# Kernel optimization log

Hardware: AMD Instinct MI355X
Metric: run time of the kernel (lower is better)

Reference implementation:

```python
import jax, jax.numpy as jnp
import numpy as np

HIDDEN = 2048
NUM_HEADS = 16
HEAD_DIM = HIDDEN // NUM_HEADS  # 128
LATENT = HIDDEN // 8            # 256
ROPE_THETA = 100000.0


def setup_inputs() -> dict:
    key = jax.random.key(0)
    ks = jax.random.split(key, 7)
    s = 0.02
    x = jax.random.normal(ks[0], (4, 1024, HIDDEN), dtype=jnp.float32)
    # weights stored as [in, out] (transpose of torch nn.Linear.weight)
    w_q_down = jax.random.normal(ks[1], (HIDDEN, LATENT), dtype=jnp.float32) * s
    w_kv_down = jax.random.normal(ks[2], (HIDDEN, LATENT), dtype=jnp.float32) * s
    w_q_up = jax.random.normal(ks[3], (LATENT, HIDDEN), dtype=jnp.float32) * s
    w_k_up = jax.random.normal(ks[4], (LATENT, HIDDEN), dtype=jnp.float32) * s
    w_v_up = jax.random.normal(ks[5], (LATENT, HIDDEN), dtype=jnp.float32) * s
    w_o = jax.random.normal(ks[6], (HIDDEN, HIDDEN), dtype=jnp.float32) * s
    return {"x": x, "w_q_down": w_q_down, "w_kv_down": w_kv_down,
            "w_q_up": w_q_up, "w_k_up": w_k_up, "w_v_up": w_v_up, "w_o": w_o}


def _rope_cos_sin(seq_len, dtype):
    # Llama rotary: inv_freq over even dims, emb = concat(freqs, freqs)
    inv_freq = 1.0 / (ROPE_THETA ** (jnp.arange(0, HEAD_DIM, 2, dtype=jnp.float32) / HEAD_DIM))
    pos = jnp.arange(seq_len, dtype=jnp.float32)
    freqs = pos[:, None] * inv_freq[None, :]          # [S, D/2]
    emb = jnp.concatenate([freqs, freqs], axis=-1)    # [S, D]
    return jnp.cos(emb).astype(dtype), jnp.sin(emb).astype(dtype)


def _rotate_half(t):
    h = t.shape[-1] // 2
    return jnp.concatenate([-t[..., h:], t[..., :h]], axis=-1)


def reference(x, w_q_down, w_kv_down, w_q_up, w_k_up, w_v_up, w_o):
    B, S, H = x.shape
    q_latent = x @ w_q_down                 # [B,S,latent]
    kv_latent = x @ w_kv_down               # [B,S,latent]
    q = (q_latent @ w_q_up).reshape(B, S, NUM_HEADS, HEAD_DIM)
    k = (kv_latent @ w_k_up).reshape(B, S, NUM_HEADS, HEAD_DIM)
    v = (kv_latent @ w_v_up).reshape(B, S, NUM_HEADS, HEAD_DIM)

    cos, sin = _rope_cos_sin(S, x.dtype)    # [S,D]
    cos = cos[None, :, None, :]             # [1,S,1,D] (unsqueeze_dim=2)
    sin = sin[None, :, None, :]
    q = q * cos + _rotate_half(q) * sin
    k = k * cos + _rotate_half(k) * sin

    # [B,H,S,D]
    q = q.transpose(0, 2, 1, 3)
    k = k.transpose(0, 2, 1, 3)
    v = v.transpose(0, 2, 1, 3)

    scale = 1.0 / jnp.sqrt(jnp.asarray(HEAD_DIM, dtype=x.dtype))
    scores = jnp.einsum('bhqd,bhkd->bhqk', q, k) * scale
    causal = jnp.tril(jnp.ones((S, S), dtype=bool))
    scores = jnp.where(causal[None, None], scores, jnp.finfo(scores.dtype).min)
    probs = jax.nn.softmax(scores, axis=-1)
    attn = jnp.einsum('bhqk,bhkd->bhqd', probs, v)  # [B,H,S,D]
    attn = attn.transpose(0, 2, 1, 3).reshape(B, S, H)
    return attn @ w_o
```

## Files before the change

### kernel.cpp

```cpp
#include <hip/hip_runtime.h>
#include <hip/hip_bf16.h>

typedef unsigned short u16;
typedef unsigned int u32;
typedef __attribute__((ext_vector_type(8))) __bf16 bf16x8;
typedef __attribute__((ext_vector_type(4))) float f32x4;

#define HID 2048
#define NH 16
#define HD 128
#define LAT 256
#define BATCH 4
#define SEQ 1024

__device__ __forceinline__ u16 f2bf(float f) {
  union { float f; u32 u; } v; v.f = f;
  u32 r = v.u + 0x7fffu + ((v.u >> 16) & 1u);
  return (u16)(r >> 16);
}

typedef const __attribute__((address_space(1))) u32 as1_u32;
typedef __attribute__((address_space(3))) u32 as3_u32;

__device__ __forceinline__ void load_lds16(const void* g, void* l) {
  __builtin_amdgcn_global_load_lds((as1_u32*)g, (as3_u32*)l, 16, 0, 0);
}

template<int WM, int WN, int MR, int NR>
__device__ __forceinline__ void gemm_core(const u16* __restrict__ A, const u16* __restrict__ Bt,
    int K, int lda, int ldb, int arow0, int brow0, u16* As, u16* Bs, f32x4 acc[MR][NR]) {
  constexpr int BM = WM * MR * 16, BN = WN * NR * 16;
  constexpr int NW = WM * WN;
  constexpr int ACH = (BM * 32) / 512;
  constexpr int BCH = (BN * 32) / 512;
  const int tid = threadIdx.x;
  const int lane = tid & 63, wave = tid >> 6;
  const int wm = wave % WM, wn = wave / WM;
  const int fr = lane & 15, fq = lane >> 4;

  for (int kt = 0; kt < K; kt += 32) {
    __syncthreads();
    #pragma unroll
    for (int cc = 0; cc < ACH / NW; ++cc) {
      int c = wave + cc * NW;
      int r = c * 16 + (lane >> 2);
      int col = (lane & 3) * 8;
      load_lds16(&A[(size_t)(arow0 + r) * lda + kt + col], &As[c * 512]);
    }
    #pragma unroll
    for (int cc = 0; cc < BCH / NW; ++cc) {
      int c = wave + cc * NW;
      int r = c * 16 + (lane >> 2);
      int col = (lane & 3) * 8;
      load_lds16(&Bt[(size_t)(brow0 + r) * ldb + kt + col], &Bs[c * 512]);
    }
    asm volatile("s_waitcnt vmcnt(0)" ::: "memory");
    __syncthreads();
    bf16x8 af[MR], bfr[NR];
    #pragma unroll
    for (int m = 0; m < MR; ++m)
      af[m] = *(const bf16x8*)&As[(wm * MR * 16 + m * 16 + fr) * 32 + fq * 8];
    #pragma unroll
    for (int n = 0; n < NR; ++n)
      bfr[n] = *(const bf16x8*)&Bs[(wn * NR * 16 + n * 16 + fr) * 32 + fq * 8];
    #pragma unroll
    for (int m = 0; m < MR; ++m)
      #pragma unroll
      for (int n = 0; n < NR; ++n)
        acc[m][n] = __builtin_amdgcn_mfma_f32_16x16x32_bf16(af[m], bfr[n], acc[m][n], 0, 0, 0);
  }
}

__global__ void __launch_bounds__(256) k_cvt(const float* __restrict__ in, u16* __restrict__ o, int n4) {
  int i = blockIdx.x * blockDim.x + threadIdx.x;
  if (i < n4) {
    float4 v = ((const float4*)in)[i];
    union { u16 s[4]; uint2 u; } w;
    w.s[0] = f2bf(v.x); w.s[1] = f2bf(v.y); w.s[2] = f2bf(v.z); w.s[3] = f2bf(v.w);
    ((uint2*)o)[i] = w.u;
  }
}

__global__ void __launch_bounds__(256) k_transpose3(const float* __restrict__ in0,
    const float* __restrict__ in1, const float* __restrict__ in2,
    u16* __restrict__ o0, u16* __restrict__ o1, u16* __restrict__ o2, int R, int C) {
  __shared__ float t[32][33];
  const float* in = blockIdx.z == 0 ? in0 : (blockIdx.z == 1 ? in1 : in2);
  u16* o = blockIdx.z == 0 ? o0 : (blockIdx.z == 1 ? o1 : o2);
  int bx = blockIdx.x * 32, by = blockIdx.y * 32;
  int tx = threadIdx.x, ty = threadIdx.y;
  #pragma unroll
  for (int i = ty; i < 32; i += 8) t[i][tx] = in[(size_t)(by + i) * C + bx + tx];
  __syncthreads();
  #pragma unroll
  for (int i = ty; i < 32; i += 8) o[(size_t)(bx + i) * R + by + tx] = f2bf(t[tx][i]);
}

__global__ void __launch_bounds__(256) k_cossin(float* __restrict__ cosT, float* __restrict__ sinT) {
  int idx = blockIdx.x * 256 + threadIdx.x;
  int s = idx >> 6, d = idx & 63;
  float inv = powf(100000.0f, -(float)d / 64.0f);
  float a = (float)s * inv;
  cosT[idx] = cosf(a);
  sinT[idx] = sinf(a);
}

__global__ void __launch_bounds__(512, 2) k_down(const u16* __restrict__ xb, const u16* __restrict__ wqdT,
    const u16* __restrict__ wkvdT, u16* __restrict__ ql, u16* __restrict__ kvl) {
  __shared__ __align__(16) u16 As[2][128 * 128];
  __shared__ __align__(16) u16 Bs[2][64 * 128];
  const u16* Bt = blockIdx.z ? wkvdT : wqdT;
  u16* out = blockIdx.z ? kvl : ql;
  const int rb = blockIdx.x * 128, cb = blockIdx.y * 64;
  const int tid = threadIdx.x, lane = tid & 63, wave = tid >> 6;
  const int wm = wave & 3, wn = wave >> 2;
  const int fr = lane & 15, fq = lane >> 4;
  const char* Ab = (const char*)xb;
  const char* Bb = (const char*)Bt;
  f32x4 acc[2][2] = {};

  auto stage = [&](int buf, int s) {
    #pragma unroll
    for (int cc = 0; cc < 4; ++cc) {
      int c = wave * 4 + cc;
      int L = c * 1024 + lane * 16;
      int Ls = L ^ (((L >> 8) & 7) << 4);
      int r = Ls >> 8, colb = Ls & 255;
      load_lds16(Ab + (size_t)(rb + r) * 4096 + s * 256 + colb, (char*)As[buf] + c * 1024);
    }
    #pragma unroll
    for (int cc = 0; cc < 2; ++cc) {
      int c = wave * 2 + cc;
      int L = c * 1024 + lane * 16;
      int Ls = L ^ (((L >> 8) & 7) << 4);
      int r = Ls >> 8, colb = Ls & 255;
      load_lds16(Bb + (size_t)(cb + r) * 4096 + s * 256 + colb, (char*)Bs[buf] + c * 1024);
    }
  };

  stage(0, 0);
  int buf = 0;
  for (int s = 0; s < 16; ++s) {
    if (s + 1 < 16) {
      stage(buf ^ 1, s + 1);
      asm volatile("s_waitcnt vmcnt(6)" ::: "memory");
    } else {
      asm volatile("s_waitcnt vmcnt(0)" ::: "memory");
    }
    asm volatile("s_barrier" ::: "memory");

    #pragma unroll
    for (int kk = 0; kk < 4; ++kk) {
      bf16x8 af[2], bfr[2];
      #pragma unroll
      for (int m = 0; m < 2; ++m) {
        int r = wm * 32 + m * 16 + fr;
        af[m] = *(const bf16x8*)((const char*)As[buf] + ((r * 256 + kk * 64 + fq * 16) ^ ((r & 7) << 4)));
      }
      #pragma unroll
      for (int n = 0; n < 2; ++n) {
        int r = wn * 32 + n * 16 + fr;
        bfr[n] = *(const bf16x8*)((const char*)Bs[buf] + ((r * 256 + kk * 64 + fq * 16) ^ ((r & 7) << 4)));
      }
      #pragma unroll
      for (int m = 0; m < 2; ++m)
        #pragma unroll
        for (int n = 0; n < 2; ++n)
          acc[m][n] = __builtin_amdgcn_mfma_f32_16x16x32_bf16(af[m], bfr[n], acc[m][n], 0, 0, 0);
    }

    asm volatile("s_barrier" ::: "memory");
    buf ^= 1;
  }

  #pragma unroll
  for (int m = 0; m < 2; ++m)
    #pragma unroll
    for (int n = 0; n < 2; ++n)
      #pragma unroll
      for (int i = 0; i < 4; ++i)
        out[(size_t)(rb + wm * 32 + m * 16 + fq * 4 + i) * LAT + cb + wn * 32 + n * 16 + fr] =
            f2bf(acc[m][n][i]);
}

__global__ void __launch_bounds__(256) k_up(const u16* __restrict__ ql, const u16* __restrict__ kvl,
    const u16* __restrict__ wquT, const u16* __restrict__ wkuT, const u16* __restrict__ wvuT,
    u16* __restrict__ q, u16* __restrict__ k, u16* __restrict__ vt,
    const float* __restrict__ cosT, const float* __restrict__ sinT) {
  __shared__ __align__(16) u16 As[128 * 32];
  __shared__ __align__(16) u16 Bs[128 * 32];
  const int mode = blockIdx.z;
  const u16* A = (mode == 0) ? ql : kvl;
  const u16* Bt = (mode == 0) ? wquT : (mode == 1 ? wkuT : wvuT);
  const int rb = blockIdx.x * 128;
  const int h = blockIdx.y;
  f32x4 acc[2][8] = {};
  gemm_core<4, 1, 2, 8>(A, Bt, LAT, LAT, LAT, rb, h * HD, As, Bs, acc);
  const int lane = threadIdx.x & 63, wave = threadIdx.x >> 6;
  const int fr = lane & 15, fq = lane >> 4;
  if (mode == 2) {
    #pragma unroll
    for (int m = 0; m < 2; ++m)
      #pragma unroll
      for (int n = 0; n < 8; ++n)
        #pragma unroll
        for (int i = 0; i < 4; ++i) {
          int row = rb + wave * 32 + m * 16 + fq * 4 + i;
          int b = row >> 10, s = row & 1023;
          int sp = (s & ~63) | (((s & 15) << 2) | ((s >> 4) & 3));
          vt[(size_t)((b * NH + h) * HD + n * 16 + fr) * SEQ + sp] = f2bf(acc[m][n][i]);
        }
  } else {
    u16* dst = (mode == 0) ? q : k;
    const float scale = (mode == 0) ? 0.08838834764831845f * 1.4426950408889634f : 1.0f;
    #pragma unroll
    for (int m = 0; m < 2; ++m)
      #pragma unroll
      for (int i = 0; i < 4; ++i) {
        int row = rb + wave * 32 + m * 16 + fq * 4 + i;
        int b = row >> 10, s = row & 1023;
        size_t base = (size_t)((b * NH + h) * SEQ + s) * HD;
        #pragma unroll
        for (int j = 0; j < 4; ++j) {
          int dlo = j * 16 + fr;
          float c = cosT[s * 64 + dlo], sn = sinT[s * 64 + dlo];
          float x1 = acc[m][j][i], x2 = acc[m][j + 4][i];
          dst[base + dlo] = f2bf((x1 * c - x2 * sn) * scale);
          dst[base + dlo + 64] = f2bf((x2 * c + x1 * sn) * scale);
        }
      }
  }
}

__global__ void __launch_bounds__(512, 2) k_attn(const u16* __restrict__ Q, const u16* __restrict__ Kc,
    const u16* __restrict__ Vt, u16* __restrict__ O) {
  __shared__ __align__(16) u16 Ks[2][64 * 128];
  __shared__ __align__(16) u16 Vs[2][128 * 64];
  __shared__ __align__(16) u16 Ps[8][16 * 64];
  const int f = blockIdx.x;
  const int bh = (f & 7) * 8 + (f >> 5);
  const int j = (f >> 3) & 3;
  const int h = bh & (NH - 1), b = bh >> 4;
  const int tid = threadIdx.x, lane = tid & 63, wave = tid >> 6;
  const int fr = lane & 15, fq = lane >> 4;
  const size_t qkb = (size_t)bh * SEQ * HD;
  const char* Kbase = (const char*)Kc + qkb * 2;
  const char* Vbase = (const char*)Vt + (size_t)bh * HD * SEQ * 2;

  const int qx0 = j, qx1 = 7 - j;
  const int nkt0 = 2 * qx0 + 2;
  const int total = 18;

  auto stage = [&](int buf, int t) {
    int kt = (t < nkt0) ? t : (t - nkt0);
    #pragma unroll
    for (int cc = 0; cc < 2; ++cc) {
      int c = wave * 2 + cc;
      int L = c * 1024 + lane * 16;
      int Lk = L ^ (((L >> 8) & 7) << 4);
      load_lds16(Kbase + (size_t)kt * 16384 + Lk, (char*)Ks[buf] + c * 1024);
      int Lv = L ^ (((L >> 7) & 7) << 4);
      int rv = Lv >> 7, colb = Lv & 127;
      load_lds16(Vbase + (size_t)rv * (SEQ * 2) + (size_t)kt * 128 + colb, (char*)Vs[buf] + c * 1024);
    }
  };

  bf16x8 ones;
  #pragma unroll
  for (int z = 0; z < 8; ++z) ones[z] = (__bf16)1.0f;

  bf16x8 qf[4];
  f32x4 ao[8];
  f32x4 lacc;
  int qw = qx0 * 128 + wave * 16;

  auto loadQ = [&]() {
    #pragma unroll
    for (int c = 0; c < 4; ++c)
      qf[c] = *(const bf16x8*)&Q[qkb + (size_t)(qw + fr) * HD + c * 32 + fq * 8];
  };
  auto reset = [&]() {
    f32x4 z = {};
    #pragma unroll
    for (int jj = 0; jj < 8; ++jj) ao[jj] = z;
    lacc = z;
  };
  auto epi = [&]() {
    #pragma unroll
    for (int i = 0; i < 4; ++i) {
      float inv = 1.f / lacc[i];
      int s = qw + fq * 4 + i;
      size_t base = (size_t)(b * SEQ + s) * HID + h * HD;
      #pragma unroll
      for (int jj = 0; jj < 8; ++jj)
        O[base + jj * 16 + fr] = f2bf(ao[jj][i] * inv);
    }
  };

  loadQ();
  reset();
  stage(0, 0);

  int cur = 0;
  for (int t = 0; t < total; ++t) {
    if (t + 1 < total) {
      stage(cur ^ 1, t + 1);
      asm volatile("s_waitcnt vmcnt(4)" ::: "memory");
    } else {
      asm volatile("s_waitcnt vmcnt(0)" ::: "memory");
    }
    asm volatile("s_barrier" ::: "memory");

    if (t == nkt0) {
      epi();
      qw = qx1 * 128 + wave * 16;
      loadQ();
      reset();
    }
    const int ktp = (t < nkt0) ? t : (t - nkt0);
    const int k0 = ktp * 64;
    if (k0 <= qw + 15) {
      f32x4 sc[4] = {};
      #pragma unroll
      for (int c = 0; c < 4; ++c)
        #pragma unroll
        for (int n = 0; n < 4; ++n) {
          int rr = n * 16 + fr;
          int off = (rr * 256 + c * 64 + fq * 16) ^ ((rr & 7) << 4);
          bf16x8 kf = *(const bf16x8*)((const char*)Ks[cur] + off);
          sc[n] = __builtin_amdgcn_mfma_f32_16x16x32_bf16(qf[c], kf, sc[n], 0, 0, 0);
        }

      const bool needmask = (k0 + 63 > qw);
      #pragma unroll
      for (int i = 0; i < 4; ++i) {
        int row = qw + fq * 4 + i;
        float p[4];
        #pragma unroll
        for (int n = 0; n < 4; ++n) {
          float sv = sc[n][i];
          if (needmask) sv = (k0 + n * 16 + fr <= row) ? sv : -1e30f;
          p[n] = exp2f(sv);
        }
        u32 w0, w1;
        asm("v_cvt_pk_bf16_f32 %0, %1, %2" : "=v"(w0) : "v"(p[0]), "v"(p[1]));
        asm("v_cvt_pk_bf16_f32 %0, %1, %2" : "=v"(w1) : "v"(p[2]), "v"(p[3]));
        int prow = fq * 4 + i;
        int o = (prow * 128 + fr * 8) ^ ((prow & 7) << 4);
        *(uint2*)((char*)Ps[wave] + o) = make_uint2(w0, w1);
      }

      bf16x8 pa[2];
      #pragma unroll
      for (int kf = 0; kf < 2; ++kf) {
        int off = (fr * 128 + kf * 64 + fq * 16) ^ ((fr & 7) << 4);
        pa[kf] = *(const bf16x8*)((const char*)Ps[wave] + off);
      }
      lacc = __builtin_amdgcn_mfma_f32_16x16x32_bf16(pa[0], ones, lacc, 0, 0, 0);
      lacc = __builtin_amdgcn_mfma_f32_16x16x32_bf16(pa[1], ones, lacc, 0, 0, 0);
      #pragma unroll
      for (int jj = 0; jj < 8; ++jj)
        #pragma unroll
        for (int kf = 0; kf < 2; ++kf) {
          int rv = jj * 16 + fr;
          int off = (rv * 128 + kf * 64 + fq * 16) ^ ((rv & 7) << 4);
          bf16x8 vf = *(const bf16x8*)((const char*)Vs[cur] + off);
          ao[jj] = __builtin_amdgcn_mfma_f32_16x16x32_bf16(pa[kf], vf, ao[jj], 0, 0, 0);
        }
    }
    asm volatile("s_barrier" ::: "memory");
    cur ^= 1;
  }
  epi();
}

__global__ void __launch_bounds__(512, 2) k_out(const u16* __restrict__ at, const u16* __restrict__ woT,
    float* __restrict__ out) {
  __shared__ __align__(16) u16 As[2][256 * 64];
  __shared__ __align__(16) u16 Bs[2][128 * 64];
  const int rb = blockIdx.x * 256, cb = blockIdx.y * 128;
  const int tid = threadIdx.x, lane = tid & 63, wave = tid >> 6;
  const int wm = wave & 3, wn = wave >> 2;
  const int fr = lane & 15, fq = lane >> 4;
  const char* Ab = (const char*)at;
  const char* Bb = (const char*)woT;
  f32x4 acc[4][4] = {};

  auto stage = [&](int buf, int s) {
    #pragma unroll
    for (int cc = 0; cc < 4; ++cc) {
      int c = wave * 4 + cc;
      int L = c * 1024 + lane * 16;
      int Ls = L ^ (((L >> 7) & 7) << 4);
      int r = Ls >> 7, colb = Ls & 127;
      load_lds16(Ab + (size_t)(rb + r) * 4096 + s * 128 + colb, (char*)As[buf] + c * 1024);
    }
    #pragma unroll
    for (int cc = 0; cc < 2; ++cc) {
      int c = wave * 2 + cc;
      int L = c * 1024 + lane * 16;
      int Ls = L ^ (((L >> 7) & 7) << 4);
      int r = Ls >> 7, colb = Ls & 127;
      load_lds16(Bb + (size_t)(cb + r) * 4096 + s * 128 + colb, (char*)Bs[buf] + c * 1024);
    }
  };

  stage(0, 0);
  int buf = 0;
  for (int s = 0; s < 32; ++s) {
    if (s + 1 < 32) {
      stage(buf ^ 1, s + 1);
      asm volatile("s_waitcnt vmcnt(6)" ::: "memory");
    } else {
      asm volatile("s_waitcnt vmcnt(0)" ::: "memory");
    }
    asm volatile("s_barrier" ::: "memory");

    #pragma unroll
    for (int kk = 0; kk < 2; ++kk) {
      bf16x8 af[4], bfr[4];
      #pragma unroll
      for (int m = 0; m < 4; ++m) {
        int r = wm * 64 + m * 16 + fr;
        af[m] = *(const bf16x8*)((const char*)As[buf] + ((r * 128 + kk * 64 + fq * 16) ^ ((r & 7) << 4)));
      }
      #pragma unroll
      for (int n = 0; n < 4; ++n) {
        int r = wn * 64 + n * 16 + fr;
        bfr[n] = *(const bf16x8*)((const char*)Bs[buf] + ((r * 128 + kk * 64 + fq * 16) ^ ((r & 7) << 4)));
      }
      #pragma unroll
      for (int m = 0; m < 4; ++m)
        #pragma unroll
        for (int n = 0; n < 4; ++n)
          acc[m][n] = __builtin_amdgcn_mfma_f32_16x16x32_bf16(af[m], bfr[n], acc[m][n], 0, 0, 0);
    }

    asm volatile("s_barrier" ::: "memory");
    buf ^= 1;
  }

  #pragma unroll
  for (int m = 0; m < 4; ++m)
    #pragma unroll
    for (int n = 0; n < 4; ++n)
      #pragma unroll
      for (int i = 0; i < 4; ++i)
        out[(size_t)(rb + wm * 64 + m * 16 + fq * 4 + i) * HID + cb + wn * 64 + n * 16 + fr] =
            acc[m][n][i];
}

extern "C" void kernel_launch(void* const* d_in, const int* in_sizes, int n_in,
                              void* d_out, int out_size, void* d_ws, size_t ws_size,
                              hipStream_t stream) {
  const float* x    = (const float*)d_in[0];
  const float* wqd  = (const float*)d_in[1];
  const float* wkvd = (const float*)d_in[2];
  const float* wqu  = (const float*)d_in[3];
  const float* wku  = (const float*)d_in[4];
  const float* wvu  = (const float*)d_in[5];
  const float* wo   = (const float*)d_in[6];
  float* out = (float*)d_out;

  char* p = (char*)d_ws;
  u16* xb    = (u16*)(p + 0);
  u16* at    = xb;
  u16* wqdT  = (u16*)(p + 16777216);
  u16* wkvdT = (u16*)(p + 17825792);
  u16* wquT  = (u16*)(p + 18874368);
  u16* wkuT  = (u16*)(p + 19922944);
  u16* wvuT  = (u16*)(p + 20971520);
  u16* woT   = (u16*)(p + 22020096);
  u16* ql    = (u16*)(p + 30408704);
  u16* kvl   = (u16*)(p + 32505856);
  u16* q     = (u16*)(p + 34603008);
  u16* kk    = (u16*)(p + 51380224);
  u16* vt    = (u16*)(p + 68157440);
  float* cosT = (float*)(p + 84934656);
  float* sinT = (float*)(p + 85196800);

  k_cvt<<<8192, 256, 0, stream>>>(x, xb, 2097152);
  k_transpose3<<<dim3(8, 64, 2), dim3(32, 8), 0, stream>>>(wqd, wkvd, wkvd, wqdT, wkvdT, wkvdT, 2048, 256);
  k_transpose3<<<dim3(64, 8, 3), dim3(32, 8), 0, stream>>>(wqu, wku, wvu, wquT, wkuT, wvuT, 256, 2048);
  k_transpose3<<<dim3(64, 64, 1), dim3(32, 8), 0, stream>>>(wo, wo, wo, woT, woT, woT, 2048, 2048);
  k_cossin<<<256, 256, 0, stream>>>(cosT, sinT);

  k_down<<<dim3(32, 4, 2), 512, 0, stream>>>(xb, wqdT, wkvdT, ql, kvl);
  k_up<<<dim3(32, 16, 3), 256, 0, stream>>>(ql, kvl, wquT, wkuT, wvuT, q, kk, vt, cosT, sinT);
  k_attn<<<256, 512, 0, stream>>>(q, kk, vt, at);
  k_out<<<dim3(16, 16), 512, 0, stream>>>(at, woT, out);
}
```

Before: 164.5 us.

## Use 32x32x16 MFMA in output GEMM with 256 threads; raise wave priority in attention MFMA

The output projection GEMM moves from 512 threads doing 16x16x32 MFMAs to 256 threads doing 32x32x16 MFMAs. Each wave now owns a 128x64 tile, and each thread issues twice as many global-to-LDS loads. This aims for better MFMA throughput and fewer fragment loads per FLOP, at the cost of more accumulator registers and less latency hiding from waves. Separately, the attention kernel wraps its MFMA sections in s_setprio(1)/s_setprio(0) so that waves doing matrix math get scheduled ahead of others.

```diff
diff --git a/kernel.cpp b/kernel.cpp
--- a/kernel.cpp
+++ b/kernel.cpp
@@ -5,6 +5,7 @@
 typedef unsigned int u32;
 typedef __attribute__((ext_vector_type(8))) __bf16 bf16x8;
 typedef __attribute__((ext_vector_type(4))) float f32x4;
+typedef __attribute__((ext_vector_type(16))) float f32x16;
 
 #define HID 2048
 #define NH 16
@@ -321,6 +322,7 @@
     const int k0 = ktp * 64;
     if (k0 <= qw + 15) {
       f32x4 sc[4] = {};
+      __builtin_amdgcn_s_setprio(1);
       #pragma unroll
       for (int c = 0; c < 4; ++c)
         #pragma unroll
@@ -330,6 +332,7 @@
           bf16x8 kf = *(const bf16x8*)((const char*)Ks[cur] + off);
           sc[n] = __builtin_amdgcn_mfma_f32_16x16x32_bf16(qf[c], kf, sc[n], 0, 0, 0);
         }
+      __builtin_amdgcn_s_setprio(0);
 
       const bool needmask = (k0 + 63 > qw);
       #pragma unroll
@@ -356,6 +359,7 @@
         int off = (fr * 128 + kf * 64 + fq * 16) ^ ((fr & 7) << 4);
         pa[kf] = *(const bf16x8*)((const char*)Ps[wave] + off);
       }
+      __builtin_amdgcn_s_setprio(1);
       lacc = __builtin_amdgcn_mfma_f32_16x16x32_bf16(pa[0], ones, lacc, 0, 0, 0);
       lacc = __builtin_amdgcn_mfma_f32_16x16x32_bf16(pa[1], ones, lacc, 0, 0, 0);
       #pragma unroll
@@ -367,6 +371,7 @@
           bf16x8 vf = *(const bf16x8*)((const char*)Vs[cur] + off);
           ao[jj] = __builtin_amdgcn_mfma_f32_16x16x32_bf16(pa[kf], vf, ao[jj], 0, 0, 0);
         }
+      __builtin_amdgcn_s_setprio(0);
     }
     asm volatile("s_barrier" ::: "memory");
     cur ^= 1;
@@ -374,33 +379,33 @@
   epi();
 }
 
-__global__ void __launch_bounds__(512, 2) k_out(const u16* __restrict__ at, const u16* __restrict__ woT,
+__global__ void __launch_bounds__(256) k_out(const u16* __restrict__ at, const u16* __restrict__ woT,
     float* __restrict__ out) {
   __shared__ __align__(16) u16 As[2][256 * 64];
   __shared__ __align__(16) u16 Bs[2][128 * 64];
   const int rb = blockIdx.x * 256, cb = blockIdx.y * 128;
   const int tid = threadIdx.x, lane = tid & 63, wave = tid >> 6;
-  const int wm = wave & 3, wn = wave >> 2;
-  const int fr = lane & 15, fq = lane >> 4;
+  const int wm = wave & 1, wn = wave >> 1;
+  const int l31 = lane & 31, lh = lane >> 5;
   const char* Ab = (const char*)at;
   const char* Bb = (const char*)woT;
-  f32x4 acc[4][4] = {};
+  f32x16 acc[4][2] = {};
 
   auto stage = [&](int buf, int s) {
+    #pragma unroll
+    for (int cc = 0; cc < 8; ++cc) {
+      int c = wave * 8 + cc;
+      int L = c * 1024 + lane * 16;
+      int Ls = L ^ (((L >> 7) & 7) << 4);
+      int r = Ls >> 7, colb = Ls & 127;
+      load_lds16(Ab + (size_t)(rb + r) * 4096 + s * 128 + colb, (char*)As[buf] + c * 1024);
+    }
     #pragma unroll
     for (int cc = 0; cc < 4; ++cc) {
       int c = wave * 4 + cc;
       int L = c * 1024 + lane * 16;
       int Ls = L ^ (((L >> 7) & 7) << 4);
       int r = Ls >> 7, colb = Ls & 127;
-      load_lds16(Ab + (size_t)(rb + r) * 4096 + s * 128 + colb, (char*)As[buf] + c * 1024);
-    }
-    #pragma unroll
-    for (int cc = 0; cc < 2; ++cc) {
-      int c = wave * 2 + cc;
-      int L = c * 1024 + lane * 16;
-      int Ls = L ^ (((L >> 7) & 7) << 4);
-      int r = Ls >> 7, colb = Ls & 127;
       load_lds16(Bb + (size_t)(cb + r) * 4096 + s * 128 + colb, (char*)Bs[buf] + c * 1024);
     }
   };
@@ -410,30 +415,32 @@
   for (int s = 0; s < 32; ++s) {
     if (s + 1 < 32) {
       stage(buf ^ 1, s + 1);
-      asm volatile("s_waitcnt vmcnt(6)" ::: "memory");
+      asm volatile("s_waitcnt vmcnt(12)" ::: "memory");
     } else {
       asm volatile("s_waitcnt vmcnt(0)" ::: "memory");
     }
     asm volatile("s_barrier" ::: "memory");
 
     #pragma unroll
-    for (int kk = 0; kk < 2; ++kk) {
-      bf16x8 af[4], bfr[4];
+    for (int ksub = 0; ksub < 4; ++ksub) {
+      bf16x8 af[4], bfr[2];
       #pragma unroll
       for (int m = 0; m < 4; ++m) {
-        int r = wm * 64 + m * 16 + fr;
-        af[m] = *(const bf16x8*)((const char*)As[buf] + ((r * 128 + kk * 64 + fq * 16) ^ ((r & 7) << 4)));
-      }
-      #pragma unroll
-      for (int n = 0; n < 4; ++n) {
-        int r = wn * 64 + n * 16 + fr;
-        bfr[n] = *(const bf16x8*)((const char*)Bs[buf] + ((r * 128 + kk * 64 + fq * 16) ^ ((r & 7) << 4)));
+        int r = wm * 128 + m * 32 + l31;
+        af[m] = *(const bf16x8*)((const char*)As[buf] +
+                 ((r * 128 + ksub * 32 + lh * 16) ^ ((r & 7) << 4)));
+      }
+      #pragma unroll
+      for (int n = 0; n < 2; ++n) {
+        int r = wn * 64 + n * 32 + l31;
+        bfr[n] = *(const bf16x8*)((const char*)Bs[buf] +
+                  ((r * 128 + ksub * 32 + lh * 16) ^ ((r & 7) << 4)));
       }
       #pragma unroll
       for (int m = 0; m < 4; ++m)
         #pragma unroll
-        for (int n = 0; n < 4; ++n)
-          acc[m][n] = __builtin_amdgcn_mfma_f32_16x16x32_bf16(af[m], bfr[n], acc[m][n], 0, 0, 0);
+        for (int n = 0; n < 2; ++n)
+          acc[m][n] = __builtin_amdgcn_mfma_f32_32x32x16_bf16(af[m], bfr[n], acc[m][n], 0, 0, 0);
     }
 
     asm volatile("s_barrier" ::: "memory");
@@ -443,11 +450,13 @@
   #pragma unroll
   for (int m = 0; m < 4; ++m)
     #pragma unroll
-    for (int n = 0; n < 4; ++n)
-      #pragma unroll
-      for (int i = 0; i < 4; ++i)
-        out[(size_t)(rb + wm * 64 + m * 16 + fq * 4 + i) * HID + cb + wn * 64 + n * 16 + fr] =
-            acc[m][n][i];
+    for (int n = 0; n < 2; ++n)
+      #pragma unroll
+      for (int reg = 0; reg < 16; ++reg) {
+        int row = rb + wm * 128 + m * 32 + (reg & 3) + 8 * (reg >> 2) + 4 * lh;
+        int col = cb + wn * 64 + n * 32 + l31;
+        out[(size_t)row * HID + col] = acc[m][n][reg];
+      }
 }
 
 extern "C" void kernel_launch(void* const* d_in, const int* in_sizes, int n_in,
@@ -488,5 +497,5 @@
   k_down<<<dim3(32, 4, 2), 512, 0, stream>>>(xb, wqdT, wkvdT, ql, kvl);
   k_up<<<dim3(32, 16, 3), 256, 0, stream>>>(ql, kvl, wquT, wkuT, wvuT, q, kk, vt, cosT, sinT);
   k_attn<<<256, 512, 0, stream>>>(q, kk, vt, at);
-  k_out<<<dim3(16, 16), 512, 0, stream>>>(at, woT, out);
-}
+  k_out<<<dim3(16, 16), 256, 0, stream>>>(at, woT, out);
+}
```

Result: slower. 171.8 us (+4.5%).
